# Kernel tuning notes

Measured on AMD Instinct MI355X. Metric: run time of the kernel, lower is better.

The kernel has to match this reference:

```python
import jax, jax.numpy as jnp
import numpy as np
import math

EMBED_DIM = 128
NUM_HEADS = 8
HDIM = EMBED_DIM // NUM_HEADS


def setup_inputs() -> dict:
    key = jax.random.key(0)
    kq, kh, km, k1, k2, k3, k4 = jax.random.split(key, 7)
    B, NQ, GS = 32, 1024, 1024
    q = jax.random.normal(kq, (B, NQ, EMBED_DIM), dtype=jnp.float32)
    h = jax.random.normal(kh, (B, GS, EMBED_DIM), dtype=jnp.float32)
    mask = jax.random.bernoulli(km, 0.15, (B, NQ, GS))
    stdv = 1.0 / math.sqrt(HDIM)
    Wq = jax.random.uniform(k1, (NUM_HEADS, EMBED_DIM, HDIM), jnp.float32, -stdv, stdv)
    Wk = jax.random.uniform(k2, (NUM_HEADS, EMBED_DIM, HDIM), jnp.float32, -stdv, stdv)
    Wv = jax.random.uniform(k3, (NUM_HEADS, EMBED_DIM, HDIM), jnp.float32, -stdv, stdv)
    stdv_o = 1.0 / math.sqrt(EMBED_DIM)
    Wout = jax.random.uniform(k4, (NUM_HEADS, HDIM, EMBED_DIM), jnp.float32, -stdv_o, stdv_o)
    return {"q": q, "h": h, "mask": mask, "Wq": Wq, "Wk": Wk, "Wv": Wv, "Wout": Wout}


def reference(q, h, mask, Wq, Wk, Wv, Wout):
    norm = 1.0 / math.sqrt(HDIM)
    # per-head projections: [h, b, n, e]
    Q = jnp.einsum('bnd,hde->hbne', q, Wq)
    K = jnp.einsum('bgd,hde->hbge', h, Wk)
    V = jnp.einsum('bgd,hde->hbge', h, Wv)
    compat = norm * jnp.einsum('hbne,hbge->hbng', Q, K)  # [h,b,nq,gs]
    m = mask[None]  # broadcast over heads
    compat = jnp.where(m, -jnp.inf, compat)
    attn = jax.nn.softmax(compat, axis=-1)
    attn = jnp.where(m, 0.0, attn)
    heads = jnp.einsum('hbng,hbge->hbne', attn, V)
    out = jnp.einsum('hbne,hed->bnd', heads, Wout)
    return out
```

## Files before the change

kernel.cpp:

```cpp
#include <hip/hip_runtime.h>

typedef unsigned short u16;
typedef unsigned int   u32;
typedef unsigned long long u64;
typedef short bf16x8 __attribute__((ext_vector_type(8)));
typedef float f32x4  __attribute__((ext_vector_type(4)));
typedef float f32x16 __attribute__((ext_vector_type(16)));

#define NB  32
#define NQ  1024
#define GS  1024
#define NH  8
#define SCQ (0.25f * 1.4426950408889634f)
#define MBIG (-1.0e30f)

#define MFMA16(a, b, c) __builtin_amdgcn_mfma_f32_16x16x32_bf16(a, b, c, 0, 0, 0)
#define MFMA32(a, b, c) __builtin_amdgcn_mfma_f32_32x32x16_bf16(a, b, c, 0, 0, 0)

__device__ __forceinline__ u16 f2bf(float f) {
    u32 u = __float_as_uint(f);
    return (u16)((u + 0x7fffu + ((u >> 16) & 1u)) >> 16);
}
__device__ __forceinline__ u32 pk2bf(float a, float b) {
    u32 ua = __float_as_uint(a) + 0x8000u;
    u32 ub = __float_as_uint(b) + 0x8000u;
    return __builtin_amdgcn_perm(ub, ua, 0x07060302u);
}

template <int MODE>
__device__ __forceinline__ void mgemm(const float* __restrict__ Ain,
                                      const float* __restrict__ Wraw,
                                      float wsc,
                                      u16* __restrict__ outb,
                                      u16* Ws, int row0) {
    const int t    = threadIdx.x;
    const int wv   = t >> 6;
    const int lane = t & 63;
    const int quad = lane >> 4;
    const int c    = lane & 15;

#pragma unroll
    for (int g0 = 0; g0 < 2048; g0 += 256) {
        int idx  = g0 + t;
        int hk   = idx >> 1, half = idx & 1;
        int k    = hk & 127;
        int col0 = (hk >> 7) * 16 + half * 8;
        const float4* wp = (const float4*)&Wraw[hk * 16 + half * 8];
        float4 w0 = wp[0], w1 = wp[1];
        Ws[(col0 + 0) * 136 + k] = f2bf(w0.x * wsc);
        Ws[(col0 + 1) * 136 + k] = f2bf(w0.y * wsc);
        Ws[(col0 + 2) * 136 + k] = f2bf(w0.z * wsc);
        Ws[(col0 + 3) * 136 + k] = f2bf(w0.w * wsc);
        Ws[(col0 + 4) * 136 + k] = f2bf(w1.x * wsc);
        Ws[(col0 + 5) * 136 + k] = f2bf(w1.y * wsc);
        Ws[(col0 + 6) * 136 + k] = f2bf(w1.z * wsc);
        Ws[(col0 + 7) * 136 + k] = f2bf(w1.w * wsc);
    }

    const float* a0p = &Ain[(size_t)(row0 + wv * 32 + c) * 128];
    const float* a1p = &Ain[(size_t)(row0 + wv * 32 + 16 + c) * 128];
    bf16x8 af0[4], af1[4];
#pragma unroll
    for (int kt = 0; kt < 4; ++kt) {
        int k0 = kt * 32 + quad * 8;
        float4 x0 = *(const float4*)&a0p[k0];
        float4 x1 = *(const float4*)&a0p[k0 + 4];
        float4 y0 = *(const float4*)&a1p[k0];
        float4 y1 = *(const float4*)&a1p[k0 + 4];
        int4 p0, p1;
        p0.x = (int)pk2bf(x0.x, x0.y);  p0.y = (int)pk2bf(x0.z, x0.w);
        p0.z = (int)pk2bf(x1.x, x1.y);  p0.w = (int)pk2bf(x1.z, x1.w);
        p1.x = (int)pk2bf(y0.x, y0.y);  p1.y = (int)pk2bf(y0.z, y0.w);
        p1.z = (int)pk2bf(y1.x, y1.y);  p1.w = (int)pk2bf(y1.z, y1.w);
        __builtin_memcpy(&af0[kt], &p0, 16);
        __builtin_memcpy(&af1[kt], &p1, 16);
    }
    __syncthreads();

    const f32x4 zf = {0.f, 0.f, 0.f, 0.f};
    f32x4 acc[2][8];
#pragma unroll
    for (int s = 0; s < 2; ++s)
#pragma unroll
        for (int j = 0; j < 8; ++j) acc[s][j] = zf;

#pragma unroll
    for (int kt = 0; kt < 4; ++kt) {
#pragma unroll
        for (int j = 0; j < 8; ++j) {
            bf16x8 bfr = *(const bf16x8*)&Ws[(j * 16 + c) * 136 + kt * 32 + quad * 8];
            acc[0][j] = MFMA16(af0[kt], bfr, acc[0][j]);
            acc[1][j] = MFMA16(af1[kt], bfr, acc[1][j]);
        }
    }

    __syncthreads();
    u16* Os = Ws;
#pragma unroll
    for (int s = 0; s < 2; ++s)
#pragma unroll
        for (int j = 0; j < 8; ++j)
#pragma unroll
            for (int r = 0; r < 4; ++r) {
                int lrow = wv * 32 + s * 16 + quad * 4 + r;
                int col  = j * 16 + c;
                u16 v = f2bf(acc[s][j][r]);
                if (MODE == 0) {
                    Os[lrow * 136 + col] = v;
                } else {
                    int u   = lrow & 15;
                    int sw  = ((u >> 2) ^ (u >> 3)) & 1;
                    int tbp = lrow ^ (sw ? 12 : 0);
                    Os[col * 136 + tbp] = v;
                }
            }
    __syncthreads();

    if (MODE == 0) {
#pragma unroll
        for (int it = 0; it < 8; ++it) {
            int chunk = it * 256 + t;
            int lrow = chunk >> 4, c0 = (chunk & 15) * 8;
            *(int4*)&outb[(size_t)(row0 + lrow) * 128 + c0] =
                *(const int4*)&Os[lrow * 136 + c0];
        }
    } else {
        int bI = row0 >> 10, tb0 = row0 & 1023;
#pragma unroll
        for (int it = 0; it < 8; ++it) {
            int chunk = it * 256 + t;
            int col = chunk >> 4, t0 = (chunk & 15) * 8;
            *(int4*)&outb[(size_t)bI * (128 * 1024) + (size_t)col * 1024 + tb0 + t0] =
                *(const int4*)&Os[col * 136 + t0];
        }
    }
}

__global__ __launch_bounds__(256, 3) void proj_mfma(const float* __restrict__ q,
                                                    const float* __restrict__ h,
                                                    const float* __restrict__ Wq,
                                                    const float* __restrict__ Wk,
                                                    const float* __restrict__ Wv,
                                                    const float* __restrict__ Wout,
                                                    u16* __restrict__ Qb,
                                                    u16* __restrict__ Kb,
                                                    u16* __restrict__ Vtg,
                                                    u16* __restrict__ Wob) {
    __shared__ u16 Ws[128 * 136];
    int y = blockIdx.y;
    if (y == 3) {
        if (blockIdx.x < 64) {
            int i = blockIdx.x * 256 + threadIdx.x;
            int d = i >> 7, he = i & 127;
            Wob[i] = f2bf(Wout[(he >> 4) * 2048 + (he & 15) * 128 + d]);
        }
        return;
    }
    int row0 = blockIdx.x * 128;
    if (y == 0)      mgemm<0>(q, Wq, SCQ,  Qb,  Ws, row0);
    else if (y == 1) mgemm<0>(h, Wk, 1.0f, Kb,  Ws, row0);
    else             mgemm<2>(h, Wv, 1.0f, Vtg, Ws, row0);
}

__global__ __launch_bounds__(512, 4) void flash_mfma(const u16* __restrict__ Qb,
                                                     const u16* __restrict__ Kb,
                                                     const u16* __restrict__ Vtg,
                                                     const int* __restrict__ mask,
                                                     const u16* __restrict__ Wob,
                                                     float* __restrict__ out) {
    __shared__ u16 Kt[64 * 136];
    __shared__ u16 Vtt[128 * 72];
    __shared__ u64 Mb[32][17];

    const int b    = blockIdx.x;
    const int q0   = blockIdx.y * 32;
    const int t    = threadIdx.x;
    const int hh   = t >> 6;
    const int lane = t & 63;
    const int quad = lane >> 4;
    const int c    = lane & 15;
    const int qq   = lane & 31;
    const int hi   = lane >> 5;

    {
        int row = t >> 4, jj = t & 15;
        const int4* mp4 = (const int4*)&mask[((size_t)b * NQ + q0 + row) * GS +
                                             jj * 64];
        u32 lo = 0, hi32 = 0;
#pragma unroll
        for (int i = 0; i < 8; ++i) {
            int4 m = mp4[i];
            u32 nib = (m.x ? 1u : 0u) | (m.y ? 2u : 0u) |
                      (m.z ? 4u : 0u) | (m.w ? 8u : 0u);
            lo |= nib << (i * 4);
        }
#pragma unroll
        for (int i = 8; i < 16; ++i) {
            int4 m = mp4[i];
            u32 nib = (m.x ? 1u : 0u) | (m.y ? 2u : 0u) |
                      (m.z ? 4u : 0u) | (m.w ? 8u : 0u);
            hi32 |= nib << ((i - 8) * 4);
        }
        Mb[row][jj] = ((u64)hi32 << 32) | lo;
    }

    bf16x8 qf = *(const bf16x8*)&Qb[((size_t)b * NQ + q0 + qq) * 128 +
                                    hh * 16 + hi * 8];

    const int skey = t >> 4;
    const int sd0  = (t & 15) * 8;
    const int vdim = t >> 2;
    const int vs0  = (t & 3) * 8;

    const u16* Kp = &Kb[((size_t)b * GS + skey) * 128 + sd0];
    const u16* Vp = &Vtg[(size_t)b * (128 * 1024) + (size_t)vdim * 1024 + vs0];

    int4 kreg0 = *(const int4*)Kp;
    int4 kreg1 = *(const int4*)(Kp + 32 * 128);
    int4 vreg0 = *(const int4*)Vp;
    int4 vreg1 = *(const int4*)(Vp + 32);

    f32x16 O32;
#pragma unroll
    for (int r = 0; r < 16; ++r) O32[r] = 0.f;
    float lsum = 0.f;
    const u32 mbb = __float_as_uint(MBIG);

    for (int g0 = 0; g0 < GS; g0 += 64) {
        __syncthreads();
        *(int4*)&Kt[skey * 136 + sd0]        = kreg0;
        *(int4*)&Kt[(32 + skey) * 136 + sd0] = kreg1;
        *(int4*)&Vtt[vdim * 72 + vs0]        = vreg0;
        *(int4*)&Vtt[vdim * 72 + 32 + vs0]   = vreg1;
        __syncthreads();

        if (g0 + 64 < GS) {
            Kp += 64 * 128;
            Vp += 64;
            kreg0 = *(const int4*)Kp;
            kreg1 = *(const int4*)(Kp + 32 * 128);
            vreg0 = *(const int4*)Vp;
            vreg1 = *(const int4*)(Vp + 32);
        }

        u64 mw  = Mb[qq][g0 >> 6];
        u32 wlo = ((u32)mw) >> (4 * hi);
        u32 whi = ((u32)(mw >> 32)) >> (4 * hi);
        f32x16 c0, c1;
#pragma unroll
        for (int r = 0; r < 16; ++r) {
            const int pos = (r & 3) + 8 * (r >> 2);
            c0[r] = __uint_as_float(((u32)(((int)(wlo << (31 - pos))) >> 31)) & mbb);
            c1[r] = __uint_as_float(((u32)(((int)(whi << (31 - pos))) >> 31)) & mbb);
        }

        bf16x8 kf0 = *(const bf16x8*)&Kt[qq * 136 + hh * 16 + hi * 8];
        bf16x8 kf1 = *(const bf16x8*)&Kt[(32 + qq) * 136 + hh * 16 + hi * 8];
        f32x16 s0 = MFMA32(kf0, qf, c0);
        f32x16 s1 = MFMA32(kf1, qf, c1);

        bf16x8 vf0 = *(const bf16x8*)&Vtt[(hh * 16 + c) * 72 + hi * 8];
        bf16x8 vf1 = *(const bf16x8*)&Vtt[(hh * 16 + c) * 72 + 16 + hi * 8];
        bf16x8 vf2 = *(const bf16x8*)&Vtt[(hh * 16 + c) * 72 + 32 + hi * 8];
        bf16x8 vf3 = *(const bf16x8*)&Vtt[(hh * 16 + c) * 72 + 48 + hi * 8];

#pragma unroll
        for (int r = 0; r < 16; ++r) s0[r] = __builtin_amdgcn_exp2f(s0[r]);
        lsum += ((s0[0] + s0[1]) + (s0[2] + s0[3])) + ((s0[4] + s0[5]) + (s0[6] + s0[7])) +
                (((s0[8] + s0[9]) + (s0[10] + s0[11])) + ((s0[12] + s0[13]) + (s0[14] + s0[15])));
        {
            int4 pa, pb;
            pa.x = (int)pk2bf(s0[0],  s0[1]);  pa.y = (int)pk2bf(s0[2],  s0[3]);
            pa.z = (int)pk2bf(s0[4],  s0[5]);  pa.w = (int)pk2bf(s0[6],  s0[7]);
            pb.x = (int)pk2bf(s0[8],  s0[9]);  pb.y = (int)pk2bf(s0[10], s0[11]);
            pb.z = (int)pk2bf(s0[12], s0[13]); pb.w = (int)pk2bf(s0[14], s0[15]);
            bf16x8 p0, p1;
            __builtin_memcpy(&p0, &pa, 16);
            __builtin_memcpy(&p1, &pb, 16);
            O32 = MFMA32(vf0, p0, O32);
            O32 = MFMA32(vf1, p1, O32);
        }

#pragma unroll
        for (int r = 0; r < 16; ++r) s1[r] = __builtin_amdgcn_exp2f(s1[r]);
        lsum += ((s1[0] + s1[1]) + (s1[2] + s1[3])) + ((s1[4] + s1[5]) + (s1[6] + s1[7])) +
                (((s1[8] + s1[9]) + (s1[10] + s1[11])) + ((s1[12] + s1[13]) + (s1[14] + s1[15])));
        {
            int4 pa, pb;
            pa.x = (int)pk2bf(s1[0],  s1[1]);  pa.y = (int)pk2bf(s1[2],  s1[3]);
            pa.z = (int)pk2bf(s1[4],  s1[5]);  pa.w = (int)pk2bf(s1[6],  s1[7]);
            pb.x = (int)pk2bf(s1[8],  s1[9]);  pb.y = (int)pk2bf(s1[10], s1[11]);
            pb.z = (int)pk2bf(s1[12], s1[13]); pb.w = (int)pk2bf(s1[14], s1[15]);
            bf16x8 p2, p3;
            __builtin_memcpy(&p2, &pa, 16);
            __builtin_memcpy(&p3, &pb, 16);
            O32 = MFMA32(vf2, p2, O32);
            O32 = MFMA32(vf3, p3, O32);
        }
    }

    lsum += __shfl_xor(lsum, 32);
    float rl = (lsum > 0.f) ? 1.f / lsum : 0.f;

    u32 h0 = pk2bf(O32[0] * rl, O32[1] * rl);
    u32 h1 = pk2bf(O32[2] * rl, O32[3] * rl);
    u32 h2 = pk2bf(O32[4] * rl, O32[5] * rl);
    u32 h3 = pk2bf(O32[6] * rl, O32[7] * rl);
    __syncthreads();
    u16* Hs = Kt;
    int2 ha; ha.x = (int)h0; ha.y = (int)h1;
    int2 hb; hb.x = (int)h2; hb.y = (int)h3;
    *(int2*)&Hs[qq * 136 + hh * 16 + 4 * hi]     = ha;
    *(int2*)&Hs[qq * 136 + hh * 16 + 8 + 4 * hi] = hb;
    __syncthreads();

    const f32x4 zf = {0.f, 0.f, 0.f, 0.f};
    f32x4 oacc[2] = {zf, zf};
#pragma unroll
    for (int kt = 0; kt < 4; ++kt) {
        bf16x8 bfr = *(const bf16x8*)&Wob[(hh * 16 + c) * 128 + kt * 32 + quad * 8];
#pragma unroll
        for (int s = 0; s < 2; ++s) {
            bf16x8 af = *(const bf16x8*)&Hs[(s * 16 + c) * 136 + kt * 32 + quad * 8];
            oacc[s] = MFMA16(af, bfr, oacc[s]);
        }
    }
#pragma unroll
    for (int s = 0; s < 2; ++s)
#pragma unroll
        for (int r = 0; r < 4; ++r)
            out[((size_t)b * NQ + q0 + s * 16 + quad * 4 + r) * 128 + hh * 16 + c] =
                oacc[s][r];
}

extern "C" void kernel_launch(void* const* d_in, const int* in_sizes, int n_in,
                              void* d_out, int out_size, void* d_ws, size_t ws_size,
                              hipStream_t stream) {
    const float* q    = (const float*)d_in[0];
    const float* h    = (const float*)d_in[1];
    const int*   mask = (const int*)d_in[2];
    const float* Wq   = (const float*)d_in[3];
    const float* Wk   = (const float*)d_in[4];
    const float* Wv   = (const float*)d_in[5];
    const float* Wout = (const float*)d_in[6];
    float* out = (float*)d_out;

    const size_t NTOK = (size_t)NB * NQ;
    u16* Qb  = (u16*)d_ws;
    u16* Kb  = Qb + NTOK * 128;
    u16* Vtg = Kb + NTOK * 128;
    u16* Wob = Vtg + NTOK * 128;

    proj_mfma<<<dim3(256, 4), 256, 0, stream>>>(q, h, Wq, Wk, Wv, Wout,
                                                Qb, Kb, Vtg, Wob);
    flash_mfma<<<dim3(NB, NQ / 32), 512, 0, stream>>>(Qb, Kb, Vtg, mask,
                                                      Wob, out);
}
```

Baseline: 299.1 us.

## Stream mask per tile into shared float bias instead of upfront bitmask

Removes the prologue that read the whole 32x1024 mask strip and packed it into a 64-bit bitmask in shared memory. Instead each iteration prefetches the next 64-column mask slice alongside K/V into registers, writes it to shared memory as float bias values (-1e30 or 0), and lanes read MFMA accumulator init values with vector LDS loads rather than shift/mask bit decoding. This overlaps mask loading with compute and cuts ALU decode work, at the cost of more LDS traffic and per-iteration global loads that use narrow int2 accesses.

Measured after the change: 276.0 us, median of 2. 7.7% less time.

```diff
diff --git a/kernel.cpp b/kernel.cpp
--- a/kernel.cpp
+++ b/kernel.cpp
@@ -2,8 +2,8 @@
 
 typedef unsigned short u16;
 typedef unsigned int   u32;
-typedef unsigned long long u64;
 typedef short bf16x8 __attribute__((ext_vector_type(8)));
+typedef float f32x2  __attribute__((ext_vector_type(2)));
 typedef float f32x4  __attribute__((ext_vector_type(4)));
 typedef float f32x16 __attribute__((ext_vector_type(16)));
 
@@ -170,7 +170,7 @@
                                                      float* __restrict__ out) {
     __shared__ u16 Kt[64 * 136];
     __shared__ u16 Vtt[128 * 72];
-    __shared__ u64 Mb[32][17];
+    __shared__ float Mf[32 * 68];
 
     const int b    = blockIdx.x;
     const int q0   = blockIdx.y * 32;
@@ -182,49 +182,31 @@
     const int qq   = lane & 31;
     const int hi   = lane >> 5;
 
-    {
-        int row = t >> 4, jj = t & 15;
-        const int4* mp4 = (const int4*)&mask[((size_t)b * NQ + q0 + row) * GS +
-                                             jj * 64];
-        u32 lo = 0, hi32 = 0;
-#pragma unroll
-        for (int i = 0; i < 8; ++i) {
-            int4 m = mp4[i];
-            u32 nib = (m.x ? 1u : 0u) | (m.y ? 2u : 0u) |
-                      (m.z ? 4u : 0u) | (m.w ? 8u : 0u);
-            lo |= nib << (i * 4);
-        }
-#pragma unroll
-        for (int i = 8; i < 16; ++i) {
-            int4 m = mp4[i];
-            u32 nib = (m.x ? 1u : 0u) | (m.y ? 2u : 0u) |
-                      (m.z ? 4u : 0u) | (m.w ? 8u : 0u);
-            hi32 |= nib << ((i - 8) * 4);
-        }
-        Mb[row][jj] = ((u64)hi32 << 32) | lo;
-    }
-
     bf16x8 qf = *(const bf16x8*)&Qb[((size_t)b * NQ + q0 + qq) * 128 +
                                     hh * 16 + hi * 8];
+
+    f32x16 O32;
+#pragma unroll
+    for (int r = 0; r < 16; ++r) O32[r] = 0.f;
+    float lsum = 0.f;
 
     const int skey = t >> 4;
     const int sd0  = (t & 15) * 8;
     const int vdim = t >> 2;
     const int vs0  = (t & 3) * 8;
-
-    const u16* Kp = &Kb[((size_t)b * GS + skey) * 128 + sd0];
-    const u16* Vp = &Vtg[(size_t)b * (128 * 1024) + (size_t)vdim * 1024 + vs0];
-
-    int4 kreg0 = *(const int4*)Kp;
-    int4 kreg1 = *(const int4*)(Kp + 32 * 128);
-    int4 vreg0 = *(const int4*)Vp;
-    int4 vreg1 = *(const int4*)(Vp + 32);
-
-    f32x16 O32;
-#pragma unroll
-    for (int r = 0; r < 16; ++r) O32[r] = 0.f;
-    float lsum = 0.f;
-    const u32 mbb = __float_as_uint(MBIG);
+    const int mrow = t >> 4;
+    const int mk0  = (t & 15) * 2;
+
+    const u16* Kptr = &Kb[((size_t)b * GS + skey) * 128 + sd0];
+    const u16* Vptr = &Vtg[(size_t)b * (128 * 1024) + (size_t)vdim * 1024 + vs0];
+    const int* Mptr = &mask[((size_t)b * NQ + q0 + mrow) * GS + mk0];
+
+    int4 kreg0 = *(const int4*)Kptr;
+    int4 kreg1 = *(const int4*)(Kptr + 32 * 128);
+    int4 vreg0 = *(const int4*)Vptr;
+    int4 vreg1 = *(const int4*)(Vptr + 32);
+    int2 mreg0 = *(const int2*)Mptr;
+    int2 mreg1 = *(const int2*)(Mptr + 32);
 
     for (int g0 = 0; g0 < GS; g0 += 64) {
         __syncthreads();
@@ -232,30 +214,39 @@
         *(int4*)&Kt[(32 + skey) * 136 + sd0] = kreg1;
         *(int4*)&Vtt[vdim * 72 + vs0]        = vreg0;
         *(int4*)&Vtt[vdim * 72 + 32 + vs0]   = vreg1;
+        f32x2 mm0, mm1;
+        mm0.x = mreg0.x ? MBIG : 0.f;
+        mm0.y = mreg0.y ? MBIG : 0.f;
+        mm1.x = mreg1.x ? MBIG : 0.f;
+        mm1.y = mreg1.y ? MBIG : 0.f;
+        *(f32x2*)&Mf[mrow * 68 + mk0]      = mm0;
+        *(f32x2*)&Mf[mrow * 68 + 32 + mk0] = mm1;
         __syncthreads();
 
         if (g0 + 64 < GS) {
-            Kp += 64 * 128;
-            Vp += 64;
-            kreg0 = *(const int4*)Kp;
-            kreg1 = *(const int4*)(Kp + 32 * 128);
-            vreg0 = *(const int4*)Vp;
-            vreg1 = *(const int4*)(Vp + 32);
-        }
-
-        u64 mw  = Mb[qq][g0 >> 6];
-        u32 wlo = ((u32)mw) >> (4 * hi);
-        u32 whi = ((u32)(mw >> 32)) >> (4 * hi);
-        f32x16 c0, c1;
-#pragma unroll
-        for (int r = 0; r < 16; ++r) {
-            const int pos = (r & 3) + 8 * (r >> 2);
-            c0[r] = __uint_as_float(((u32)(((int)(wlo << (31 - pos))) >> 31)) & mbb);
-            c1[r] = __uint_as_float(((u32)(((int)(whi << (31 - pos))) >> 31)) & mbb);
+            Kptr += 64 * 128;
+            kreg0 = *(const int4*)Kptr;
+            kreg1 = *(const int4*)(Kptr + 32 * 128);
+            Vptr += 64;
+            vreg0 = *(const int4*)Vptr;
+            vreg1 = *(const int4*)(Vptr + 32);
+            Mptr += 64;
+            mreg0 = *(const int2*)Mptr;
+            mreg1 = *(const int2*)(Mptr + 32);
         }
 
         bf16x8 kf0 = *(const bf16x8*)&Kt[qq * 136 + hh * 16 + hi * 8];
         bf16x8 kf1 = *(const bf16x8*)&Kt[(32 + qq) * 136 + hh * 16 + hi * 8];
+        f32x16 c0, c1;
+#pragma unroll
+        for (int blk = 0; blk < 4; ++blk) {
+            f32x4 m0 = *(const f32x4*)&Mf[qq * 68 + 8 * blk + 4 * hi];
+            f32x4 m1 = *(const f32x4*)&Mf[qq * 68 + 32 + 8 * blk + 4 * hi];
+            c0[4 * blk + 0] = m0.x;  c0[4 * blk + 1] = m0.y;
+            c0[4 * blk + 2] = m0.z;  c0[4 * blk + 3] = m0.w;
+            c1[4 * blk + 0] = m1.x;  c1[4 * blk + 1] = m1.y;
+            c1[4 * blk + 2] = m1.z;  c1[4 * blk + 3] = m1.w;
+        }
         f32x16 s0 = MFMA32(kf0, qf, c0);
         f32x16 s1 = MFMA32(kf1, qf, c1);
 
```
